# Kernel optimization log

Measured on AMD Instinct MI355X. Metric: run time of the kernel, lower is better.

## Reference

```python
import jax, jax.numpy as jnp
import numpy as np

TAU = 0.65
NUM_NEG = 10
N, M, D, K = 200000, 200000, 128, 5


def setup_inputs() -> dict:
    key = jax.random.key(0)
    k1, k2, k3, k4 = jax.random.split(key, 4)
    return {
        "embeddings": jax.random.normal(k1, (N, D), dtype=jnp.float32),
        "negative_embs": jax.random.normal(k2, (M, D), dtype=jnp.float32),
        "community_pos_options": jax.random.randint(k3, (N, K), 0, N),
        "neg_idx": jax.random.randint(k4, (NUM_NEG, N), 0, M),
        "iter_n": 3,
    }


def reference(embeddings, negative_embs, community_pos_options, neg_idx, iter_n):
    # positive example per node: embeddings[community_pos_options[:, iter_n-1]] -> [N, D]
    pos = embeddings[community_pos_options[:, iter_n - 1]]
    # gathered negatives: [NUM_NEG, N, D] (irregular gather)
    negs = negative_embs[neg_idx]
    # original detaches the left-hand embedding inside compute_mutual_info_score
    e = jax.lax.stop_gradient(embeddings)
    # numerator: per-node dot(embedding, positive) / tau -> [N]
    num = jnp.einsum("nd,nd->n", e, pos) / TAU
    # denominator logits: all_samples = [positive] + 10 negatives -> [N, 1+NUM_NEG]
    neg_logits = jnp.einsum("nd,knd->nk", e, negs) / TAU
    logits = jnp.concatenate([num[:, None], neg_logits], axis=1)
    # score = logsumexp(denominator) - numerator, mean over nodes
    score = jax.nn.logsumexp(logits, axis=1) - num
    return score.mean()
```

## Files before the change

### kernel.cpp

```cpp
#include <hip/hip_runtime.h>
#include <hip/hip_bf16.h>
#include <hip/hip_fp16.h>


#define TAU_F     0.65f
#define NUM_NEG   10
#define K_OPT     5

typedef _Float16 half8  __attribute__((ext_vector_type(8)));
typedef _Float16 half2v __attribute__((ext_vector_type(2)));
typedef float    f32x4  __attribute__((ext_vector_type(4)));

#if __has_builtin(__builtin_amdgcn_cvt_pk_f32_fp8) && __has_builtin(__builtin_amdgcn_cvt_pk_fp8_f32)
#define NEGFP8 1
#else
#define NEGFP8 0
#endif

__device__ inline float dot8(half8 a, half8 b, float c) {
#if __has_builtin(__builtin_amdgcn_fdot2)
    half2v a0 = {a[0], a[1]}, b0 = {b[0], b[1]};
    half2v a1 = {a[2], a[3]}, b1 = {b[2], b[3]};
    half2v a2 = {a[4], a[5]}, b2 = {b[4], b[5]};
    half2v a3 = {a[6], a[7]}, b3 = {b[6], b[7]};
    c = __builtin_amdgcn_fdot2(a0, b0, c, false);
    c = __builtin_amdgcn_fdot2(a1, b1, c, false);
    c = __builtin_amdgcn_fdot2(a2, b2, c, false);
    c = __builtin_amdgcn_fdot2(a3, b3, c, false);
#else
#pragma unroll
    for (int j = 0; j < 8; ++j) c += (float)a[j] * (float)b[j];
#endif
    return c;
}

__global__ __launch_bounds__(256) void cl_convert(
    const f32x4* __restrict__ srcA, const f32x4* __restrict__ srcB,
    half8* __restrict__ dstA, void* __restrict__ dstB_,
    int nA8, int nB8)
{
    int i = blockIdx.x * blockDim.x + threadIdx.x;
    const int stride = gridDim.x * blockDim.x;
    const int total = nA8 + nB8;
    for (; i < total; i += stride) {
        if (i < nA8) {
            const int j = i;
            const f32x4 a = __builtin_nontemporal_load(srcA + 2 * j);
            const f32x4 b = __builtin_nontemporal_load(srcA + 2 * j + 1);
            half8 h;
            h[0] = (_Float16)a.x; h[1] = (_Float16)a.y;
            h[2] = (_Float16)a.z; h[3] = (_Float16)a.w;
            h[4] = (_Float16)b.x; h[5] = (_Float16)b.y;
            h[6] = (_Float16)b.z; h[7] = (_Float16)b.w;
            dstA[j] = h;
        } else {
            const int j = i - nA8;
            const f32x4 a = __builtin_nontemporal_load(srcB + 2 * j);
            const f32x4 b = __builtin_nontemporal_load(srcB + 2 * j + 1);
#if NEGFP8
            int w0 = __builtin_amdgcn_cvt_pk_fp8_f32(a.x, a.y, 0, false);
            w0     = __builtin_amdgcn_cvt_pk_fp8_f32(a.z, a.w, w0, true);
            int w1 = __builtin_amdgcn_cvt_pk_fp8_f32(b.x, b.y, 0, false);
            w1     = __builtin_amdgcn_cvt_pk_fp8_f32(b.z, b.w, w1, true);
            ((uint2*)dstB_)[j] = make_uint2((unsigned)w0, (unsigned)w1);
#else
            half8 h;
            h[0] = (_Float16)a.x; h[1] = (_Float16)a.y;
            h[2] = (_Float16)a.z; h[3] = (_Float16)a.w;
            h[4] = (_Float16)b.x; h[5] = (_Float16)b.y;
            h[6] = (_Float16)b.z; h[7] = (_Float16)b.w;
            ((half8*)dstB_)[j] = h;
#endif
        }
    }
}

__global__ __launch_bounds__(256) void cl_rows_q(
    const half8* __restrict__ emb16,
    const void*  __restrict__ negtab_,
    const int*   __restrict__ posopt,
    const int*   __restrict__ negidx,
    const int*   __restrict__ iter_n,
    float*       __restrict__ partials,
    int N)
{
    const int tid  = threadIdx.x;
    const int lane = tid & 15;
    const int gpb  = blockDim.x >> 4;
    const int g0   = blockIdx.x * gpb + (tid >> 4);
    const int gstr = gridDim.x * gpb;
    const int col  = iter_n[0] - 1;
    const float inv_tau = 1.0f / TAU_F;

#if NEGFP8
    const uint2* __restrict__ neg8 = (const uint2*)negtab_;
#else
    const half8* __restrict__ neg16 = (const half8*)negtab_;
#endif

    float local = 0.0f;

    for (int row = g0; row < N; row += gstr) {
        const half8 e = emb16[row * 16 + lane];

        float acc[NUM_NEG + 1];
        {
            const int pidx = posopt[row * K_OPT + col];
            acc[0] = dot8(e, emb16[pidx * 16 + lane], 0.0f);
        }

#if NEGFP8
        float ef[8];
#pragma unroll
        for (int j = 0; j < 8; ++j) ef[j] = (float)e[j];
#endif

#pragma unroll
        for (int k = 0; k < NUM_NEG; ++k) {
            const int j = negidx[k * N + row];
#if NEGFP8
            const uint2 w = neg8[j * 16 + lane];
            const auto p0 = __builtin_amdgcn_cvt_pk_f32_fp8(w.x, false);
            const auto p1 = __builtin_amdgcn_cvt_pk_f32_fp8(w.x, true);
            const auto p2 = __builtin_amdgcn_cvt_pk_f32_fp8(w.y, false);
            const auto p3 = __builtin_amdgcn_cvt_pk_f32_fp8(w.y, true);
            float c;
            c = ef[0] * p0[0];
            c = fmaf(ef[1], p0[1], c);
            c = fmaf(ef[2], p1[0], c);
            c = fmaf(ef[3], p1[1], c);
            c = fmaf(ef[4], p2[0], c);
            c = fmaf(ef[5], p2[1], c);
            c = fmaf(ef[6], p3[0], c);
            c = fmaf(ef[7], p3[1], c);
            acc[k + 1] = c;
#else
            acc[k + 1] = dot8(e, neg16[j * 16 + lane], 0.0f);
#endif
        }

#pragma unroll
        for (int m = 1; m < 16; m <<= 1) {
#pragma unroll
            for (int k = 0; k < NUM_NEG + 1; ++k)
                acc[k] += __shfl_xor(acc[k], m, 64);
        }

        const float num = acc[0] * inv_tau;
        float mx = num;
        float l[NUM_NEG];
#pragma unroll
        for (int k = 0; k < NUM_NEG; ++k) {
            l[k] = acc[k + 1] * inv_tau;
            mx = fmaxf(mx, l[k]);
        }
        float s = expf(num - mx);
#pragma unroll
        for (int k = 0; k < NUM_NEG; ++k) s += expf(l[k] - mx);
        const float score = mx + logf(s) - num;

        if (lane == 0) local += score;
    }

#pragma unroll
    for (int m = 1; m < 64; m <<= 1) local += __shfl_xor(local, m, 64);

    __shared__ float sm[8];
    const int wave = tid >> 6;
    if ((tid & 63) == 0) sm[wave] = local;
    __syncthreads();
    if (tid == 0) {
        float t = 0.0f;
        const int nw = blockDim.x >> 6;
        for (int w = 0; w < nw; ++w) t += sm[w];
        partials[blockIdx.x] = t;
    }
}

__global__ __launch_bounds__(256) void cl_rows_f32(
    const float* __restrict__ emb, const float* __restrict__ negemb,
    const int* __restrict__ posopt, const int* __restrict__ negidx,
    const int* __restrict__ iter_n, float* __restrict__ partials, int N)
{
    const int tid  = threadIdx.x;
    const int sub  = tid & 31;
    const int hpb  = blockDim.x >> 5;
    const int h0   = blockIdx.x * hpb + (tid >> 5);
    const int hstr = gridDim.x * hpb;
    const int col  = iter_n[0] - 1;
    const float4* emb4 = reinterpret_cast<const float4*>(emb);
    const float4* neg4 = reinterpret_cast<const float4*>(negemb);
    const float inv_tau = 1.0f / TAU_F;
    float local = 0.0f;
    for (int row = h0; row < N; row += hstr) {
        const float4 e = emb4[row * 32 + sub];
        float acc[NUM_NEG + 1];
        {
            const int pidx = posopt[row * K_OPT + col];
            const float4 p = emb4[pidx * 32 + sub];
            acc[0] = e.x * p.x + e.y * p.y + e.z * p.z + e.w * p.w;
        }
#pragma unroll
        for (int k = 0; k < NUM_NEG; ++k) {
            const int j = negidx[k * N + row];
            const float4 v = neg4[j * 32 + sub];
            acc[k + 1] = e.x * v.x + e.y * v.y + e.z * v.z + e.w * v.w;
        }
#pragma unroll
        for (int m = 1; m < 32; m <<= 1)
#pragma unroll
            for (int k = 0; k < NUM_NEG + 1; ++k)
                acc[k] += __shfl_xor(acc[k], m, 64);
        const float num = acc[0] * inv_tau;
        float mx = num;
        float l[NUM_NEG];
#pragma unroll
        for (int k = 0; k < NUM_NEG; ++k) { l[k] = acc[k + 1] * inv_tau; mx = fmaxf(mx, l[k]); }
        float s = expf(num - mx);
#pragma unroll
        for (int k = 0; k < NUM_NEG; ++k) s += expf(l[k] - mx);
        const float score = mx + logf(s) - num;
        if (sub == 0) local += score;
    }
#pragma unroll
    for (int m = 1; m < 64; m <<= 1) local += __shfl_xor(local, m, 64);
    __shared__ float sm[8];
    const int wave = tid >> 6;
    if ((tid & 63) == 0) sm[wave] = local;
    __syncthreads();
    if (tid == 0) {
        float t = 0.0f;
        for (int w = 0; w < (int)(blockDim.x >> 6); ++w) t += sm[w];
        partials[blockIdx.x] = t;
    }
}

__global__ __launch_bounds__(256) void cl_finish(
    const float* __restrict__ partials, int nb, float* __restrict__ out, float invN)
{
    __shared__ float sm[256];
    float t = 0.0f;
    for (int i = threadIdx.x; i < nb; i += 256) t += partials[i];
    sm[threadIdx.x] = t;
    __syncthreads();
    for (int s = 128; s > 0; s >>= 1) {
        if (threadIdx.x < s) sm[threadIdx.x] += sm[threadIdx.x + s];
        __syncthreads();
    }
    if (threadIdx.x == 0) out[0] = sm[0] * invN;
}

extern "C" void kernel_launch(void* const* d_in, const int* in_sizes, int n_in,
                              void* d_out, int out_size, void* d_ws, size_t ws_size,
                              hipStream_t stream) {
    const float* emb    = (const float*)d_in[0];
    const float* negemb = (const float*)d_in[1];
    const int*   posopt = (const int*)d_in[2];
    const int*   negidx = (const int*)d_in[3];
    const int*   itern  = (const int*)d_in[4];
    float*       out    = (float*)d_out;

    const int elemsA = in_sizes[0];
    const int elemsB = in_sizes[1];
    const int N      = in_sizes[3] / NUM_NEG;

    const int nblocks = 2048;

    const size_t bytesA = (size_t)elemsA * 2;
#if NEGFP8
    const size_t bytesB = (size_t)elemsB * 1;
#else
    const size_t bytesB = (size_t)elemsB * 2;
#endif
    size_t poff = (bytesA + bytesB + 255) & ~(size_t)255;
    const size_t needed = poff + (size_t)nblocks * sizeof(float);

    if (ws_size >= needed) {
        half8* dstA = (half8*)d_ws;
        void*  dstB = (void*)((char*)d_ws + bytesA);
        float* partials = (float*)((char*)d_ws + poff);

        cl_convert<<<2048, 256, 0, stream>>>(
            (const f32x4*)emb, (const f32x4*)negemb,
            dstA, dstB, elemsA / 8, elemsB / 8);
        cl_rows_q<<<nblocks, 256, 0, stream>>>(
            dstA, dstB, posopt, negidx, itern, partials, N);
        cl_finish<<<1, 256, 0, stream>>>(partials, nblocks, out, 1.0f / (float)N);
    } else {
        int nb = nblocks;
        const int max_parts = (int)(ws_size / sizeof(float));
        if (nb > max_parts) nb = max_parts;
        float* partials = (float*)d_ws;
        cl_rows_f32<<<nb, 256, 0, stream>>>(emb, negemb, posopt, negidx, itern,
                                            partials, N);
        cl_finish<<<1, 256, 0, stream>>>(partials, nb, out, 1.0f / (float)N);
    }
}
```

Baseline: 114.7 us.

## Quantize embeddings to FP8 and assign contiguous row ranges per group

The embedding table, used for the self rows and the positive gathers, is now stored in FP8 like the negatives instead of FP16. This halves its footprint and the bytes fetched per row and per positive gather. The conversion kernel is merged into one branch-free path for both tables. Each 16-lane group now walks a contiguous block of rows rather than a grid-strided sequence, which changes the access pattern for the row and index reads. The trade is lower precision on both operands of every dot product.

```diff
diff --git a/kernel.cpp b/kernel.cpp
--- a/kernel.cpp
+++ b/kernel.cpp
@@ -12,9 +12,9 @@
 typedef float    f32x4  __attribute__((ext_vector_type(4)));
 
 #if __has_builtin(__builtin_amdgcn_cvt_pk_f32_fp8) && __has_builtin(__builtin_amdgcn_cvt_pk_fp8_f32)
-#define NEGFP8 1
-#else
-#define NEGFP8 0
+#define FP8Q 1
+#else
+#define FP8Q 0
 #endif
 
 __device__ inline float dot8(half8 a, half8 b, float c) {
@@ -34,110 +34,122 @@
     return c;
 }
 
+#if FP8Q
+__device__ inline float dotq(const float* __restrict__ ef, uint2 w) {
+    const auto p0 = __builtin_amdgcn_cvt_pk_f32_fp8(w.x, false);
+    const auto p1 = __builtin_amdgcn_cvt_pk_f32_fp8(w.x, true);
+    const auto p2 = __builtin_amdgcn_cvt_pk_f32_fp8(w.y, false);
+    const auto p3 = __builtin_amdgcn_cvt_pk_f32_fp8(w.y, true);
+    float c;
+    c = ef[0] * p0[0];
+    c = fmaf(ef[1], p0[1], c);
+    c = fmaf(ef[2], p1[0], c);
+    c = fmaf(ef[3], p1[1], c);
+    c = fmaf(ef[4], p2[0], c);
+    c = fmaf(ef[5], p2[1], c);
+    c = fmaf(ef[6], p3[0], c);
+    c = fmaf(ef[7], p3[1], c);
+    return c;
+}
+#endif
+
 __global__ __launch_bounds__(256) void cl_convert(
     const f32x4* __restrict__ srcA, const f32x4* __restrict__ srcB,
-    half8* __restrict__ dstA, void* __restrict__ dstB_,
+    void* __restrict__ dstA_, void* __restrict__ dstB_,
     int nA8, int nB8)
 {
     int i = blockIdx.x * blockDim.x + threadIdx.x;
     const int stride = gridDim.x * blockDim.x;
     const int total = nA8 + nB8;
     for (; i < total; i += stride) {
-        if (i < nA8) {
-            const int j = i;
-            const f32x4 a = __builtin_nontemporal_load(srcA + 2 * j);
-            const f32x4 b = __builtin_nontemporal_load(srcA + 2 * j + 1);
-            half8 h;
-            h[0] = (_Float16)a.x; h[1] = (_Float16)a.y;
-            h[2] = (_Float16)a.z; h[3] = (_Float16)a.w;
-            h[4] = (_Float16)b.x; h[5] = (_Float16)b.y;
-            h[6] = (_Float16)b.z; h[7] = (_Float16)b.w;
-            dstA[j] = h;
-        } else {
-            const int j = i - nA8;
-            const f32x4 a = __builtin_nontemporal_load(srcB + 2 * j);
-            const f32x4 b = __builtin_nontemporal_load(srcB + 2 * j + 1);
-#if NEGFP8
-            int w0 = __builtin_amdgcn_cvt_pk_fp8_f32(a.x, a.y, 0, false);
-            w0     = __builtin_amdgcn_cvt_pk_fp8_f32(a.z, a.w, w0, true);
-            int w1 = __builtin_amdgcn_cvt_pk_fp8_f32(b.x, b.y, 0, false);
-            w1     = __builtin_amdgcn_cvt_pk_fp8_f32(b.z, b.w, w1, true);
-            ((uint2*)dstB_)[j] = make_uint2((unsigned)w0, (unsigned)w1);
-#else
-            half8 h;
-            h[0] = (_Float16)a.x; h[1] = (_Float16)a.y;
-            h[2] = (_Float16)a.z; h[3] = (_Float16)a.w;
-            h[4] = (_Float16)b.x; h[5] = (_Float16)b.y;
-            h[6] = (_Float16)b.z; h[7] = (_Float16)b.w;
-            ((half8*)dstB_)[j] = h;
-#endif
-        }
+        const bool inA = (i < nA8);
+        const f32x4* s = inA ? srcA : srcB;
+        const int j = inA ? i : (i - nA8);
+        const f32x4 a = __builtin_nontemporal_load(s + 2 * j);
+        const f32x4 b = __builtin_nontemporal_load(s + 2 * j + 1);
+#if FP8Q
+        int w0 = __builtin_amdgcn_cvt_pk_fp8_f32(a.x, a.y, 0, false);
+        w0     = __builtin_amdgcn_cvt_pk_fp8_f32(a.z, a.w, w0, true);
+        int w1 = __builtin_amdgcn_cvt_pk_fp8_f32(b.x, b.y, 0, false);
+        w1     = __builtin_amdgcn_cvt_pk_fp8_f32(b.z, b.w, w1, true);
+        uint2* d = inA ? (uint2*)dstA_ : (uint2*)dstB_;
+        d[j] = make_uint2((unsigned)w0, (unsigned)w1);
+#else
+        half8 h;
+        h[0] = (_Float16)a.x; h[1] = (_Float16)a.y;
+        h[2] = (_Float16)a.z; h[3] = (_Float16)a.w;
+        h[4] = (_Float16)b.x; h[5] = (_Float16)b.y;
+        h[6] = (_Float16)b.z; h[7] = (_Float16)b.w;
+        half8* d = inA ? (half8*)dstA_ : (half8*)dstB_;
+        d[j] = h;
+#endif
     }
 }
 
 __global__ __launch_bounds__(256) void cl_rows_q(
-    const half8* __restrict__ emb16,
-    const void*  __restrict__ negtab_,
-    const int*   __restrict__ posopt,
-    const int*   __restrict__ negidx,
-    const int*   __restrict__ iter_n,
-    float*       __restrict__ partials,
+    const void* __restrict__ embtab_,
+    const void* __restrict__ negtab_,
+    const int*  __restrict__ posopt,
+    const int*  __restrict__ negidx,
+    const int*  __restrict__ iter_n,
+    float*      __restrict__ partials,
     int N)
 {
     const int tid  = threadIdx.x;
     const int lane = tid & 15;
     const int gpb  = blockDim.x >> 4;
-    const int g0   = blockIdx.x * gpb + (tid >> 4);
-    const int gstr = gridDim.x * gpb;
+    const int gid  = blockIdx.x * gpb + (tid >> 4);
+    const int ngroups = gridDim.x * gpb;
+    const int rpg  = (N + ngroups - 1) / ngroups;
+    const int r0   = gid * rpg;
+    const int r1   = min(N, r0 + rpg);
     const int col  = iter_n[0] - 1;
     const float inv_tau = 1.0f / TAU_F;
 
-#if NEGFP8
+#if FP8Q
+    const uint2* __restrict__ emb8 = (const uint2*)embtab_;
     const uint2* __restrict__ neg8 = (const uint2*)negtab_;
 #else
+    const half8* __restrict__ emb16 = (const half8*)embtab_;
     const half8* __restrict__ neg16 = (const half8*)negtab_;
 #endif
 
     float local = 0.0f;
 
-    for (int row = g0; row < N; row += gstr) {
+    for (int row = r0; row < r1; ++row) {
+        float acc[NUM_NEG + 1];
+#if FP8Q
+        const uint2 ew = emb8[row * 16 + lane];
+        float ef[8];
+        {
+            const auto e0 = __builtin_amdgcn_cvt_pk_f32_fp8(ew.x, false);
+            const auto e1 = __builtin_amdgcn_cvt_pk_f32_fp8(ew.x, true);
+            const auto e2 = __builtin_amdgcn_cvt_pk_f32_fp8(ew.y, false);
+            const auto e3 = __builtin_amdgcn_cvt_pk_f32_fp8(ew.y, true);
+            ef[0] = e0[0]; ef[1] = e0[1]; ef[2] = e1[0]; ef[3] = e1[1];
+            ef[4] = e2[0]; ef[5] = e2[1]; ef[6] = e3[0]; ef[7] = e3[1];
+        }
+        {
+            const int pidx = posopt[row * K_OPT + col];
+            acc[0] = dotq(ef, emb8[pidx * 16 + lane]);
+        }
+#pragma unroll
+        for (int k = 0; k < NUM_NEG; ++k) {
+            const int j = negidx[k * N + row];
+            acc[k + 1] = dotq(ef, neg8[j * 16 + lane]);
+        }
+#else
         const half8 e = emb16[row * 16 + lane];
-
-        float acc[NUM_NEG + 1];
         {
             const int pidx = posopt[row * K_OPT + col];
             acc[0] = dot8(e, emb16[pidx * 16 + lane], 0.0f);
         }
-
-#if NEGFP8
-        float ef[8];
-#pragma unroll
-        for (int j = 0; j < 8; ++j) ef[j] = (float)e[j];
-#endif
-
 #pragma unroll
         for (int k = 0; k < NUM_NEG; ++k) {
             const int j = negidx[k * N + row];
-#if NEGFP8
-            const uint2 w = neg8[j * 16 + lane];
-            const auto p0 = __builtin_amdgcn_cvt_pk_f32_fp8(w.x, false);
-            const auto p1 = __builtin_amdgcn_cvt_pk_f32_fp8(w.x, true);
-            const auto p2 = __builtin_amdgcn_cvt_pk_f32_fp8(w.y, false);
-            const auto p3 = __builtin_amdgcn_cvt_pk_f32_fp8(w.y, true);
-            float c;
-            c = ef[0] * p0[0];
-            c = fmaf(ef[1], p0[1], c);
-            c = fmaf(ef[2], p1[0], c);
-            c = fmaf(ef[3], p1[1], c);
-            c = fmaf(ef[4], p2[0], c);
-            c = fmaf(ef[5], p2[1], c);
-            c = fmaf(ef[6], p3[0], c);
-            c = fmaf(ef[7], p3[1], c);
-            acc[k + 1] = c;
-#else
             acc[k + 1] = dot8(e, neg16[j * 16 + lane], 0.0f);
-#endif
-        }
+        }
+#endif
 
 #pragma unroll
         for (int m = 1; m < 16; m <<= 1) {
@@ -266,17 +278,18 @@
 
     const int nblocks = 2048;
 
+#if FP8Q
+    const size_t bytesA = (size_t)elemsA * 1;
+    const size_t bytesB = (size_t)elemsB * 1;
+#else
     const size_t bytesA = (size_t)elemsA * 2;
-#if NEGFP8
-    const size_t bytesB = (size_t)elemsB * 1;
-#else
     const size_t bytesB = (size_t)elemsB * 2;
 #endif
     size_t poff = (bytesA + bytesB + 255) & ~(size_t)255;
     const size_t needed = poff + (size_t)nblocks * sizeof(float);
 
     if (ws_size >= needed) {
-        half8* dstA = (half8*)d_ws;
+        void*  dstA = d_ws;
         void*  dstB = (void*)((char*)d_ws + bytesA);
         float* partials = (float*)((char*)d_ws + poff);
 
```

Result: faster. 110.9 us (-3.3%).
